# Kernel optimization log

Measured on AMD Instinct MI355X. Metric: run time of the kernel, lower is better.

## Reference

```python
import jax, jax.numpy as jnp
import numpy as np

HIDDEN = 32
N_FEAT = 10  # 5 stats + 1 comprehension_delta + 4 neuromods
EPS = 1e-8
MOMENTUM_DECAY = 0.9


def setup_inputs() -> dict:
    key = jax.random.key(0)
    ks = jax.random.split(key, 12)
    grad = jax.random.normal(ks[0], (4096, 8192), dtype=jnp.float32)
    param = jax.random.normal(ks[1], (4096, 8192), dtype=jnp.float32)
    neuromod = jax.random.normal(ks[2], (4,), dtype=jnp.float32)
    comp_delta = jax.random.normal(ks[3], (1,), dtype=jnp.float32) * 0.1
    # per-parameter-group state (fresh -> zeros, matching _get_state/_get_momentum)
    m_prev = jnp.zeros((1,), dtype=jnp.float32)
    h_prev = jnp.zeros((1, HIDDEN), dtype=jnp.float32)
    c_prev = jnp.zeros((1, HIDDEN), dtype=jnp.float32)
    s = 0.1
    W_ih = jax.random.normal(ks[4], (4 * HIDDEN, N_FEAT), dtype=jnp.float32) * s
    W_hh = jax.random.normal(ks[5], (4 * HIDDEN, HIDDEN), dtype=jnp.float32) * s
    b_ih = jax.random.normal(ks[6], (4 * HIDDEN,), dtype=jnp.float32) * s
    b_hh = jax.random.normal(ks[7], (4 * HIDDEN,), dtype=jnp.float32) * s
    Ws = jax.random.normal(ks[8], (1, HIDDEN), dtype=jnp.float32) * s
    bs = jnp.zeros((1,), dtype=jnp.float32)
    Wg1 = jax.random.normal(ks[9], (HIDDEN // 2, HIDDEN), dtype=jnp.float32) * s
    bg1 = jax.random.normal(ks[10], (HIDDEN // 2,), dtype=jnp.float32) * s
    Wg2 = jax.random.normal(ks[11], (1, HIDDEN // 2), dtype=jnp.float32) * s
    bg2 = jnp.zeros((1,), dtype=jnp.float32)
    return dict(grad=grad, param=param, neuromod=neuromod, comp_delta=comp_delta,
                m_prev=m_prev, h_prev=h_prev, c_prev=c_prev,
                W_ih=W_ih, W_hh=W_hh, b_ih=b_ih, b_hh=b_hh,
                Ws=Ws, bs=bs, Wg1=Wg1, bg1=bg1, Wg2=Wg2, bg2=bg2)


def _forward(grad, param, neuromod, comp_delta, m_prev, h_prev, c_prev,
             W_ih, W_hh, b_ih, b_hh, Ws, bs, Wg1, bg1, Wg2, bg2):
    # --- four full-tensor reductions (memory-bound) ---
    g_norm = jnp.maximum(jnp.sqrt(jnp.sum(grad * grad)), EPS)
    p_norm = jnp.maximum(jnp.sqrt(jnp.sum(param * param)), EPS)
    log_g = jnp.log(g_norm + EPS).reshape(1)
    log_p = jnp.log(p_norm + EPS).reshape(1)
    cos_sim = (jnp.sum(grad * param) / (g_norm * p_norm + EPS)).reshape(1)
    signed_log_g = jnp.mean(jnp.sign(grad) * jnp.log1p(jnp.abs(grad))).reshape(1)
    momentum = (MOMENTUM_DECAY * m_prev + (1.0 - MOMENTUM_DECAY) * g_norm).reshape(1)
    # --- feature vector (1, 10) ---
    features = jnp.concatenate([log_g, log_p, cos_sim, signed_log_g,
                                momentum, comp_delta, neuromod.reshape(-1)])[None, :]
    # --- LSTMCell (torch gate order: i, f, g, o) ---
    gates = features @ W_ih.T + b_ih + h_prev @ W_hh.T + b_hh  # (1, 4H)
    i, f, g, o = jnp.split(gates, 4, axis=-1)
    c_new = jax.nn.sigmoid(f) * c_prev + jax.nn.sigmoid(i) * jnp.tanh(g)
    h_new = jax.nn.sigmoid(o) * jnp.tanh(c_new)
    # --- heads ---
    raw_scale = h_new @ Ws.T + bs                      # (1, 1)
    scale = jnp.exp(jnp.tanh(raw_scale)).squeeze()
    hid = jnp.tanh(h_new @ Wg1.T + bg1)                # (1, H/2)
    comp_g = jax.nn.sigmoid(hid @ Wg2.T + bg2).squeeze()
    mult = jnp.clip(scale * (0.5 + comp_g), 0.01, 10.0)
    return mult


def reference(grad, param, neuromod, comp_delta, m_prev, h_prev, c_prev,
              W_ih, W_hh, b_ih, b_hh, Ws, bs, Wg1, bg1, Wg2, bg2):
    return _forward(grad, param, neuromod, comp_delta, m_prev, h_prev, c_prev,
                    W_ih, W_hh, b_ih, b_hh, Ws, bs, Wg1, bg1, Wg2, bg2)
```

## Files before the change

kernel.cpp:

```cpp
#include <hip/hip_runtime.h>
#include <math.h>

#define HID 32
#define EPSF 1e-8f
#define LN2F 0.69314718055994530942f

typedef float vfloat4 __attribute__((ext_vector_type(4)));

__device__ __forceinline__ float wave_red64(float v) {
#pragma unroll
    for (int off = 32; off > 0; off >>= 1) v += __shfl_down(v, off);
    return v;
}

__device__ __forceinline__ float sigmf(float x) { return 1.0f / (1.0f + expf(-x)); }

__device__ __forceinline__ float slog2(float x) {
    return copysignf(__log2f(1.0f + fabsf(x)), x);
}

__global__ __launch_bounds__(256) void lb_reduce(
    const vfloat4* __restrict__ g4, const vfloat4* __restrict__ p4,
    float* __restrict__ partials, int n4)
{
    const int stride = gridDim.x * blockDim.x;
    const int tid = blockIdx.x * blockDim.x + threadIdx.x;

    float sg2 = 0.f, sp2 = 0.f, sgp = 0.f, ssl = 0.f;

    int i = tid;
    for (; i + 3 * stride < n4; i += 4 * stride) {
        vfloat4 g0 = __builtin_nontemporal_load(&g4[i]);
        vfloat4 g1 = __builtin_nontemporal_load(&g4[i + stride]);
        vfloat4 g2 = __builtin_nontemporal_load(&g4[i + 2 * stride]);
        vfloat4 g3 = __builtin_nontemporal_load(&g4[i + 3 * stride]);
        vfloat4 p0 = __builtin_nontemporal_load(&p4[i]);
        vfloat4 p1 = __builtin_nontemporal_load(&p4[i + stride]);
        vfloat4 p2 = __builtin_nontemporal_load(&p4[i + 2 * stride]);
        vfloat4 p3 = __builtin_nontemporal_load(&p4[i + 3 * stride]);

#define ACC(g, p)                                                                      \
        sg2 = fmaf(g.x, g.x, fmaf(g.y, g.y, fmaf(g.z, g.z, fmaf(g.w, g.w, sg2))));    \
        sp2 = fmaf(p.x, p.x, fmaf(p.y, p.y, fmaf(p.z, p.z, fmaf(p.w, p.w, sp2))));    \
        sgp = fmaf(g.x, p.x, fmaf(g.y, p.y, fmaf(g.z, p.z, fmaf(g.w, p.w, sgp))));    \
        ssl += slog2(g.x) + slog2(g.y) + slog2(g.z) + slog2(g.w);

        ACC(g0, p0)
        ACC(g1, p1)
        ACC(g2, p2)
        ACC(g3, p3)
    }
    for (; i < n4; i += stride) {
        vfloat4 g0 = __builtin_nontemporal_load(&g4[i]);
        vfloat4 p0 = __builtin_nontemporal_load(&p4[i]);
        ACC(g0, p0)
    }
#undef ACC

    sg2 = wave_red64(sg2);
    sp2 = wave_red64(sp2);
    sgp = wave_red64(sgp);
    ssl = wave_red64(ssl);
    __shared__ float sh[4][4];
    int wid = threadIdx.x >> 6;
    if ((threadIdx.x & 63) == 0) {
        sh[0][wid] = sg2; sh[1][wid] = sp2; sh[2][wid] = sgp; sh[3][wid] = ssl;
    }
    __syncthreads();
    if (threadIdx.x == 0) {
        float* out = partials + (size_t)blockIdx.x * 4;
        out[0] = sh[0][0] + sh[0][1] + sh[0][2] + sh[0][3];
        out[1] = sh[1][0] + sh[1][1] + sh[1][2] + sh[1][3];
        out[2] = sh[2][0] + sh[2][1] + sh[2][2] + sh[2][3];
        out[3] = sh[3][0] + sh[3][1] + sh[3][2] + sh[3][3];
    }
}

__global__ __launch_bounds__(256) void lb_finish(
    const float* __restrict__ partials, int nblk,
    const float* __restrict__ neuromod, const float* __restrict__ comp_delta,
    const float* __restrict__ m_prev, const float* __restrict__ h_prev,
    const float* __restrict__ c_prev,
    const float* __restrict__ W_ih, const float* __restrict__ W_hh,
    const float* __restrict__ b_ih, const float* __restrict__ b_hh,
    const float* __restrict__ Ws, const float* __restrict__ bs,
    const float* __restrict__ Wg1, const float* __restrict__ bg1,
    const float* __restrict__ Wg2, const float* __restrict__ bg2,
    float* __restrict__ out, float sl_scale )
{
    __shared__ float feat[10];
    __shared__ float gates[4 * HID];
    __shared__ float hnew[HID];
    __shared__ float hidv[HID / 2];
    __shared__ float shred[4][4];

    float s0 = 0.f, s1 = 0.f, s2 = 0.f, s3 = 0.f;
    for (int i = threadIdx.x; i < nblk; i += blockDim.x) {
        const float* p = partials + (size_t)i * 4;
        s0 += p[0]; s1 += p[1]; s2 += p[2]; s3 += p[3];
    }
    s0 = wave_red64(s0); s1 = wave_red64(s1); s2 = wave_red64(s2); s3 = wave_red64(s3);
    int wid = threadIdx.x >> 6;
    if ((threadIdx.x & 63) == 0) {
        shred[0][wid] = s0; shred[1][wid] = s1; shred[2][wid] = s2; shred[3][wid] = s3;
    }
    __syncthreads();

    if (threadIdx.x == 0) {
        float sum_g2 = shred[0][0] + shred[0][1] + shred[0][2] + shred[0][3];
        float sum_p2 = shred[1][0] + shred[1][1] + shred[1][2] + shred[1][3];
        float sum_gp = shred[2][0] + shred[2][1] + shred[2][2] + shred[2][3];
        float sum_sl = shred[3][0] + shred[3][1] + shred[3][2] + shred[3][3];
        float g_norm = fmaxf(sqrtf(sum_g2), EPSF);
        float p_norm = fmaxf(sqrtf(sum_p2), EPSF);
        feat[0] = logf(g_norm + EPSF);
        feat[1] = logf(p_norm + EPSF);
        feat[2] = sum_gp / (g_norm * p_norm + EPSF);
        feat[3] = sum_sl * sl_scale;
        feat[4] = 0.9f * m_prev[0] + (1.0f - 0.9f) * g_norm;
        feat[5] = comp_delta[0];
        feat[6] = neuromod[0];
        feat[7] = neuromod[1];
        feat[8] = neuromod[2];
        feat[9] = neuromod[3];
    }
    __syncthreads();

    if (threadIdx.x < 4 * HID) {
        int r = threadIdx.x;
        float acc = b_ih[r] + b_hh[r];
#pragma unroll
        for (int k = 0; k < 10; ++k) acc = fmaf(W_ih[r * 10 + k], feat[k], acc);
#pragma unroll
        for (int k = 0; k < HID; ++k) acc = fmaf(W_hh[r * HID + k], h_prev[k], acc);
        gates[r] = acc;
    }
    __syncthreads();

    if (threadIdx.x < HID) {
        int j = threadIdx.x;
        float iv = sigmf(gates[j]);
        float fv = sigmf(gates[HID + j]);
        float gv = tanhf(gates[2 * HID + j]);
        float ov = sigmf(gates[3 * HID + j]);
        float c = fv * c_prev[j] + iv * gv;
        hnew[j] = ov * tanhf(c);
    }
    __syncthreads();

    if (threadIdx.x < HID / 2) {
        int k = threadIdx.x;
        float a = bg1[k];
#pragma unroll
        for (int j = 0; j < HID; ++j) a = fmaf(Wg1[k * HID + j], hnew[j], a);
        hidv[k] = tanhf(a);
    }
    __syncthreads();

    if (threadIdx.x == 0) {
        float rs = bs[0];
#pragma unroll
        for (int j = 0; j < HID; ++j) rs = fmaf(Ws[j], hnew[j], rs);
        float scale = expf(tanhf(rs));
        float cg = bg2[0];
#pragma unroll
        for (int k = 0; k < HID / 2; ++k) cg = fmaf(Wg2[k], hidv[k], cg);
        float comp_g = sigmf(cg);
        float mult = scale * (0.5f + comp_g);
        mult = fminf(fmaxf(mult, 0.01f), 10.0f);
        out[0] = mult;
    }
}

extern "C" void kernel_launch(void* const* d_in, const int* in_sizes, int n_in,
                              void* d_out, int out_size, void* d_ws, size_t ws_size,
                              hipStream_t stream) {
    const float* grad       = (const float*)d_in[0];
    const float* param      = (const float*)d_in[1];
    const float* neuromod   = (const float*)d_in[2];
    const float* comp_delta = (const float*)d_in[3];
    const float* m_prev     = (const float*)d_in[4];
    const float* h_prev     = (const float*)d_in[5];
    const float* c_prev     = (const float*)d_in[6];
    const float* W_ih       = (const float*)d_in[7];
    const float* W_hh       = (const float*)d_in[8];
    const float* b_ih       = (const float*)d_in[9];
    const float* b_hh       = (const float*)d_in[10];
    const float* Ws         = (const float*)d_in[11];
    const float* bs         = (const float*)d_in[12];
    const float* Wg1        = (const float*)d_in[13];
    const float* bg1        = (const float*)d_in[14];
    const float* Wg2        = (const float*)d_in[15];
    const float* bg2        = (const float*)d_in[16];

    int n = in_sizes[0];
    int n4 = n / 4;

    int nblk = 2048;
    size_t need = (size_t)nblk * 4 * sizeof(float);
    if (ws_size < need) {
        nblk = (int)(ws_size / (4 * sizeof(float)));
        if (nblk < 1) nblk = 1;
    }
    float* partials = (float*)d_ws;

    lb_reduce<<<nblk, 256, 0, stream>>>((const vfloat4*)grad, (const vfloat4*)param,
                                        partials, n4);
    lb_finish<<<1, 256, 0, stream>>>(partials, nblk,
                                     neuromod, comp_delta, m_prev, h_prev, c_prev,
                                     W_ih, W_hh, b_ih, b_hh, Ws, bs,
                                     Wg1, bg1, Wg2, bg2,
                                     (float*)d_out, LN2F / (float)n);
}
```

Baseline: 58.41 us.

## Fuse reduction and LSTM head into one kernel via last-block atomic counter

Merges the two-kernel reduce-then-finish design into one kernel. Each block writes its partial sums, then increments an atomic counter, and the last block to arrive does the final reduction and the small LSTM/head computation. This removes a second kernel launch but adds a hipMemsetAsync to reset the counter. Alongside, the main loop drops nontemporal loads and goes from 4x unrolling to 2x with split accumulators, which may change how much memory is in flight.

```diff
diff --git a/kernel.cpp b/kernel.cpp
--- a/kernel.cpp
+++ b/kernel.cpp
@@ -19,65 +19,10 @@
     return copysignf(__log2f(1.0f + fabsf(x)), x);
 }
 
-__global__ __launch_bounds__(256) void lb_reduce(
+__global__ __launch_bounds__(256) void lb_fused(
     const vfloat4* __restrict__ g4, const vfloat4* __restrict__ p4,
-    float* __restrict__ partials, int n4)
-{
-    const int stride = gridDim.x * blockDim.x;
-    const int tid = blockIdx.x * blockDim.x + threadIdx.x;
-
-    float sg2 = 0.f, sp2 = 0.f, sgp = 0.f, ssl = 0.f;
-
-    int i = tid;
-    for (; i + 3 * stride < n4; i += 4 * stride) {
-        vfloat4 g0 = __builtin_nontemporal_load(&g4[i]);
-        vfloat4 g1 = __builtin_nontemporal_load(&g4[i + stride]);
-        vfloat4 g2 = __builtin_nontemporal_load(&g4[i + 2 * stride]);
-        vfloat4 g3 = __builtin_nontemporal_load(&g4[i + 3 * stride]);
-        vfloat4 p0 = __builtin_nontemporal_load(&p4[i]);
-        vfloat4 p1 = __builtin_nontemporal_load(&p4[i + stride]);
-        vfloat4 p2 = __builtin_nontemporal_load(&p4[i + 2 * stride]);
-        vfloat4 p3 = __builtin_nontemporal_load(&p4[i + 3 * stride]);
-
-#define ACC(g, p)                                                                      \
-        sg2 = fmaf(g.x, g.x, fmaf(g.y, g.y, fmaf(g.z, g.z, fmaf(g.w, g.w, sg2))));    \
-        sp2 = fmaf(p.x, p.x, fmaf(p.y, p.y, fmaf(p.z, p.z, fmaf(p.w, p.w, sp2))));    \
-        sgp = fmaf(g.x, p.x, fmaf(g.y, p.y, fmaf(g.z, p.z, fmaf(g.w, p.w, sgp))));    \
-        ssl += slog2(g.x) + slog2(g.y) + slog2(g.z) + slog2(g.w);
-
-        ACC(g0, p0)
-        ACC(g1, p1)
-        ACC(g2, p2)
-        ACC(g3, p3)
-    }
-    for (; i < n4; i += stride) {
-        vfloat4 g0 = __builtin_nontemporal_load(&g4[i]);
-        vfloat4 p0 = __builtin_nontemporal_load(&p4[i]);
-        ACC(g0, p0)
-    }
-#undef ACC
-
-    sg2 = wave_red64(sg2);
-    sp2 = wave_red64(sp2);
-    sgp = wave_red64(sgp);
-    ssl = wave_red64(ssl);
-    __shared__ float sh[4][4];
-    int wid = threadIdx.x >> 6;
-    if ((threadIdx.x & 63) == 0) {
-        sh[0][wid] = sg2; sh[1][wid] = sp2; sh[2][wid] = sgp; sh[3][wid] = ssl;
-    }
-    __syncthreads();
-    if (threadIdx.x == 0) {
-        float* out = partials + (size_t)blockIdx.x * 4;
-        out[0] = sh[0][0] + sh[0][1] + sh[0][2] + sh[0][3];
-        out[1] = sh[1][0] + sh[1][1] + sh[1][2] + sh[1][3];
-        out[2] = sh[2][0] + sh[2][1] + sh[2][2] + sh[2][3];
-        out[3] = sh[3][0] + sh[3][1] + sh[3][2] + sh[3][3];
-    }
-}
-
-__global__ __launch_bounds__(256) void lb_finish(
-    const float* __restrict__ partials, int nblk,
+    float* __restrict__ partials, unsigned* __restrict__ counter,
+    int n4,
     const float* __restrict__ neuromod, const float* __restrict__ comp_delta,
     const float* __restrict__ m_prev, const float* __restrict__ h_prev,
     const float* __restrict__ c_prev,
@@ -88,29 +33,83 @@
     const float* __restrict__ Wg2, const float* __restrict__ bg2,
     float* __restrict__ out, float sl_scale )
 {
+    const int stride = gridDim.x * blockDim.x;
+    const int tid = blockIdx.x * blockDim.x + threadIdx.x;
+
+    float sg2a = 0.f, sp2a = 0.f, sgpa = 0.f, ssla = 0.f;
+    float sg2b = 0.f, sp2b = 0.f, sgpb = 0.f, sslb = 0.f;
+
+#define ACC(g, p, sg2, sp2, sgp, ssl)                                                  \
+        sg2 = fmaf(g.x, g.x, fmaf(g.y, g.y, fmaf(g.z, g.z, fmaf(g.w, g.w, sg2))));    \
+        sp2 = fmaf(p.x, p.x, fmaf(p.y, p.y, fmaf(p.z, p.z, fmaf(p.w, p.w, sp2))));    \
+        sgp = fmaf(g.x, p.x, fmaf(g.y, p.y, fmaf(g.z, p.z, fmaf(g.w, p.w, sgp))));    \
+        ssl += slog2(g.x) + slog2(g.y) + slog2(g.z) + slog2(g.w);
+
+    int i = tid;
+    for (; i + stride < n4; i += 2 * stride) {
+        vfloat4 g0 = g4[i];
+        vfloat4 p0 = p4[i];
+        vfloat4 g1 = g4[i + stride];
+        vfloat4 p1 = p4[i + stride];
+        ACC(g0, p0, sg2a, sp2a, sgpa, ssla)
+        ACC(g1, p1, sg2b, sp2b, sgpb, sslb)
+    }
+    for (; i < n4; i += stride) {
+        vfloat4 g0 = g4[i];
+        vfloat4 p0 = p4[i];
+        ACC(g0, p0, sg2a, sp2a, sgpa, ssla)
+    }
+#undef ACC
+
+    float sg2 = wave_red64(sg2a + sg2b);
+    float sp2 = wave_red64(sp2a + sp2b);
+    float sgp = wave_red64(sgpa + sgpb);
+    float ssl = wave_red64(ssla + sslb);
+
+    __shared__ float sh[4][4];
+    const int wid = threadIdx.x >> 6;
+    if ((threadIdx.x & 63) == 0) {
+        sh[0][wid] = sg2; sh[1][wid] = sp2; sh[2][wid] = sgp; sh[3][wid] = ssl;
+    }
+    __syncthreads();
+
+    __shared__ bool amLast;
+    if (threadIdx.x == 0) {
+        float* o = partials + (size_t)blockIdx.x * 4;
+        o[0] = sh[0][0] + sh[0][1] + sh[0][2] + sh[0][3];
+        o[1] = sh[1][0] + sh[1][1] + sh[1][2] + sh[1][3];
+        o[2] = sh[2][0] + sh[2][1] + sh[2][2] + sh[2][3];
+        o[3] = sh[3][0] + sh[3][1] + sh[3][2] + sh[3][3];
+        __threadfence();
+        unsigned old = atomicAdd(counter, 1u);
+        amLast = (old == gridDim.x - 1);
+    }
+    __syncthreads();
+    if (!amLast) return;
+    __threadfence();
+
     __shared__ float feat[10];
     __shared__ float gates[4 * HID];
     __shared__ float hnew[HID];
     __shared__ float hidv[HID / 2];
-    __shared__ float shred[4][4];
-
+
+    const int nblk = gridDim.x;
     float s0 = 0.f, s1 = 0.f, s2 = 0.f, s3 = 0.f;
-    for (int i = threadIdx.x; i < nblk; i += blockDim.x) {
-        const float* p = partials + (size_t)i * 4;
+    for (int b = threadIdx.x; b < nblk; b += blockDim.x) {
+        const float* p = partials + (size_t)b * 4;
         s0 += p[0]; s1 += p[1]; s2 += p[2]; s3 += p[3];
     }
     s0 = wave_red64(s0); s1 = wave_red64(s1); s2 = wave_red64(s2); s3 = wave_red64(s3);
-    int wid = threadIdx.x >> 6;
     if ((threadIdx.x & 63) == 0) {
-        shred[0][wid] = s0; shred[1][wid] = s1; shred[2][wid] = s2; shred[3][wid] = s3;
+        sh[0][wid] = s0; sh[1][wid] = s1; sh[2][wid] = s2; sh[3][wid] = s3;
     }
     __syncthreads();
 
     if (threadIdx.x == 0) {
-        float sum_g2 = shred[0][0] + shred[0][1] + shred[0][2] + shred[0][3];
-        float sum_p2 = shred[1][0] + shred[1][1] + shred[1][2] + shred[1][3];
-        float sum_gp = shred[2][0] + shred[2][1] + shred[2][2] + shred[2][3];
-        float sum_sl = shred[3][0] + shred[3][1] + shred[3][2] + shred[3][3];
+        float sum_g2 = sh[0][0] + sh[0][1] + sh[0][2] + sh[0][3];
+        float sum_p2 = sh[1][0] + sh[1][1] + sh[1][2] + sh[1][3];
+        float sum_gp = sh[2][0] + sh[2][1] + sh[2][2] + sh[2][3];
+        float sum_sl = sh[3][0] + sh[3][1] + sh[3][2] + sh[3][3];
         float g_norm = fmaxf(sqrtf(sum_g2), EPSF);
         float p_norm = fmaxf(sqrtf(sum_p2), EPSF);
         feat[0] = logf(g_norm + EPSF);
@@ -197,18 +196,20 @@
     int n4 = n / 4;
 
     int nblk = 2048;
-    size_t need = (size_t)nblk * 4 * sizeof(float);
+    size_t need = (size_t)nblk * 4 * sizeof(float) + sizeof(unsigned);
     if (ws_size < need) {
-        nblk = (int)(ws_size / (4 * sizeof(float)));
+        nblk = (int)((ws_size - sizeof(unsigned)) / (4 * sizeof(float)));
         if (nblk < 1) nblk = 1;
     }
-    float* partials = (float*)d_ws;
-
-    lb_reduce<<<nblk, 256, 0, stream>>>((const vfloat4*)grad, (const vfloat4*)param,
-                                        partials, n4);
-    lb_finish<<<1, 256, 0, stream>>>(partials, nblk,
-                                     neuromod, comp_delta, m_prev, h_prev, c_prev,
-                                     W_ih, W_hh, b_ih, b_hh, Ws, bs,
-                                     Wg1, bg1, Wg2, bg2,
-                                     (float*)d_out, LN2F / (float)n);
-}
+    float* partials  = (float*)d_ws;
+    unsigned* counter = (unsigned*)((char*)d_ws + (size_t)nblk * 4 * sizeof(float));
+
+    hipMemsetAsync(counter, 0, sizeof(unsigned), stream);
+
+    lb_fused<<<nblk, 256, 0, stream>>>((const vfloat4*)grad, (const vfloat4*)param,
+                                       partials, counter, n4,
+                                       neuromod, comp_delta, m_prev, h_prev, c_prev,
+                                       W_ih, W_hh, b_ih, b_hh, Ws, bs,
+                                       Wg1, bg1, Wg2, bg2,
+                                       (float*)d_out, LN2F / (float)n);
+}
```

New measurement: 119.1 us. +103.9%, slower.
